# Optimization experiments

Hardware: AMD Instinct MI355X
Metric: run time of the kernel (lower is better)

The kernel has to match this reference:

```python
import jax, jax.numpy as jnp
import numpy as np

B, T, N, HID = 64, 24, 184, 128
IN2 = 2  # 2 * in_dim


def setup_inputs() -> dict:
    key = jax.random.key(0)
    ks = jax.random.split(key, 7)
    s = 1.0 / np.sqrt(HID)
    return {
        "pm25_hist": jax.random.normal(ks[0], (B, T, N, 1), dtype=jnp.float32),
        "W_ih": jax.random.uniform(ks[1], (3 * HID, IN2), dtype=jnp.float32, minval=-s, maxval=s),
        "W_hh": jax.random.uniform(ks[2], (3 * HID, HID), dtype=jnp.float32, minval=-s, maxval=s),
        "b_ih": jax.random.uniform(ks[3], (3 * HID,), dtype=jnp.float32, minval=-s, maxval=s),
        "b_hh": jax.random.uniform(ks[4], (3 * HID,), dtype=jnp.float32, minval=-s, maxval=s),
        "fc_w": jax.random.uniform(ks[5], (1, HID), dtype=jnp.float32, minval=-s, maxval=s),
        "fc_b": jax.random.uniform(ks[6], (1,), dtype=jnp.float32, minval=-s, maxval=s),
    }


def _encoder(pm25_hist, W_ih, W_hh, b_ih, b_hh, fc_w, fc_b):
    b, t, n, _ = pm25_hist.shape
    hid = W_hh.shape[1]
    h0 = jnp.zeros((b * n, hid), dtype=pm25_hist.dtype)
    x0 = jnp.zeros((b, n, 1), dtype=pm25_hist.dtype)
    xs = jnp.transpose(pm25_hist, (1, 0, 2, 3))  # [T, B, N, 1]

    def step(carry, pm_t):
        hn, xn = carry
        x = jnp.concatenate([xn, pm_t], axis=-1).reshape(b * n, -1)  # [B*N, 2]
        gi = x @ W_ih.T + b_ih      # [B*N, 3H]
        gh = hn @ W_hh.T + b_hh     # [B*N, 3H]
        i_r, i_z, i_n = jnp.split(gi, 3, axis=-1)
        h_r, h_z, h_n = jnp.split(gh, 3, axis=-1)
        r = jax.nn.sigmoid(i_r + h_r)
        z = jax.nn.sigmoid(i_z + h_z)
        nt = jnp.tanh(i_n + r * h_n)
        h_new = (1.0 - z) * nt + z * hn
        Ht = h_new.reshape(b, n, hid)
        x_new = Ht @ fc_w.T + fc_b  # [B, N, 1]
        return (h_new, x_new), Ht

    (_, xn_final), H = jax.lax.scan(step, (h0, x0), xs)
    H = jnp.transpose(H, (1, 0, 2, 3))  # [B, T, N, HID]
    return H, xn_final


def reference(pm25_hist, W_ih, W_hh, b_ih, b_hh, fc_w, fc_b):
    return _encoder(pm25_hist, W_ih, W_hh, b_ih, b_hh, fc_w, fc_b)
```

## Files before the change

kernel.cpp:

```cpp
#include <hip/hip_runtime.h>
#include <hip/hip_fp16.h>


#define B_   64
#define T_   24
#define N_   184
#define H_   128
#define BN   (B_ * N_)
#define TN   (T_ * N_)
#define HSZ  (B_ * T_ * N_ * H_)
#define MROWS 16
#define NBLK  (BN / MROWS)
#define S16   136

typedef _Float16 v8h __attribute__((ext_vector_type(8)));
typedef float    v4f __attribute__((ext_vector_type(4)));

static __device__ __forceinline__ float fast_rcp(float x) {
#if __has_builtin(__builtin_amdgcn_rcpf)
    return __builtin_amdgcn_rcpf(x);
#else
    return 1.0f / x;
#endif
}
static __device__ __forceinline__ float sigm_f(float x) {
    return fast_rcp(1.0f + __expf(-x));
}
static __device__ __forceinline__ float tanh_f(float x) {
    return 1.0f - 2.0f * fast_rcp(1.0f + __expf(2.0f * x));
}

__global__ __launch_bounds__(256, 2)
void gru_encoder_kernel(const float* __restrict__ pm,
                        const float* __restrict__ Wih,
                        const float* __restrict__ Whh,
                        const float* __restrict__ bih,
                        const float* __restrict__ bhh,
                        const float* __restrict__ fcw,
                        const float* __restrict__ fcb,
                        float* __restrict__ out)
{
    __shared__ _Float16 hf[MROWS * S16];
    __shared__ float    pml[T_ * MROWS];
    __shared__ float    xlds[MROWS];
    __shared__ float    xpart[4 * MROWS];

    const int tid  = threadIdx.x;
    const int w    = tid >> 6;
    const int lane = tid & 63;
    const int u    = lane & 15;
    const int q    = lane >> 4;

    for (int idx = tid; idx < MROWS * S16; idx += 256) hf[idx] = (_Float16)0.0f;
    if (tid < MROWS) xlds[tid] = 0.0f;

    for (int idx = tid; idx < T_ * MROWS; idx += 256) {
        const int row = idx & (MROWS - 1);
        const int t   = idx >> 4;
        const int g   = blockIdx.x * MROWS + row;
        const int b   = g / N_;
        const int n   = g - b * N_;
        pml[t * MROWS + row] = pm[b * TN + t * N_ + n];
    }

    v8h bfr[3][2][4];
#pragma unroll
    for (int g = 0; g < 3; ++g)
#pragma unroll
        for (int p = 0; p < 2; ++p) {
            const int n = g * 128 + (2 * w + p) * 16 + u;
#pragma unroll
            for (int ks = 0; ks < 4; ++ks) {
                const float* src = Whh + n * 128 + ks * 32 + q * 8;
                v8h hb;
#pragma unroll
                for (int j = 0; j < 8; ++j) hb[j] = (_Float16)src[j];
                bfr[g][p][ks] = hb;
            }
        }

    float w0[3][2], w1[3][2], brz0[2], brz1[2], bin_[2], bhn_[2], fcwr[2];
#pragma unroll
    for (int p = 0; p < 2; ++p) {
        const int i = (2 * w + p) * 16 + u;
        w0[0][p] = Wih[(0 * 128 + i) * 2 + 0];  w1[0][p] = Wih[(0 * 128 + i) * 2 + 1];
        w0[1][p] = Wih[(1 * 128 + i) * 2 + 0];  w1[1][p] = Wih[(1 * 128 + i) * 2 + 1];
        w0[2][p] = Wih[(2 * 128 + i) * 2 + 0];  w1[2][p] = Wih[(2 * 128 + i) * 2 + 1];
        brz0[p] = bih[0 * 128 + i] + bhh[0 * 128 + i];
        brz1[p] = bih[1 * 128 + i] + bhh[1 * 128 + i];
        bin_[p] = bih[2 * 128 + i];
        bhn_[p] = bhh[2 * 128 + i];
        fcwr[p] = fcw[i];
    }
    const float fcbv = fcb[0];

    int obase[4];
#pragma unroll
    for (int reg = 0; reg < 4; ++reg) {
        const int g = blockIdx.x * MROWS + q * 4 + reg;
        const int b = g / N_;
        obase[reg] = b * TN + (g - b * N_);
    }

    v4f hreg[2];
    hreg[0] = (v4f){0.f, 0.f, 0.f, 0.f};
    hreg[1] = (v4f){0.f, 0.f, 0.f, 0.f};

    __syncthreads();

    for (int t = 0; t < T_; ++t) {
        v4f acc[3][2];
#pragma unroll
        for (int g = 0; g < 3; ++g)
#pragma unroll
            for (int p = 0; p < 2; ++p) acc[g][p] = (v4f){0.f, 0.f, 0.f, 0.f};

#pragma unroll
        for (int ks = 0; ks < 4; ++ks) {
            const v8h afr = *(const v8h*)&hf[u * S16 + ks * 32 + q * 8];
#pragma unroll
            for (int g = 0; g < 3; ++g)
#pragma unroll
                for (int p = 0; p < 2; ++p)
                    acc[g][p] = __builtin_amdgcn_mfma_f32_16x16x32_f16(
                        afr, bfr[g][p][ks], acc[g][p], 0, 0, 0);
        }
        __syncthreads();

        const int tN = t * N_;
#pragma unroll
        for (int reg = 0; reg < 4; ++reg) {
            const int lr  = q * 4 + reg;
            const int ob  = obase[reg] + tN;
            const float xp  = xlds[lr];
            const float pmv = pml[t * MROWS + lr];
            float xsum = 0.0f;
#pragma unroll
            for (int p = 0; p < 2; ++p) {
                const int i = (2 * w + p) * 16 + u;
                const float r  = sigm_f(xp * w0[0][p] + pmv * w1[0][p] + acc[0][p][reg] + brz0[p]);
                const float z  = sigm_f(xp * w0[1][p] + pmv * w1[1][p] + acc[1][p][reg] + brz1[p]);
                const float nt = tanh_f(xp * w0[2][p] + pmv * w1[2][p] + bin_[p] +
                                        r * (acc[2][p][reg] + bhn_[p]));
                const float hnew = (1.0f - z) * nt + z * hreg[p][reg];
                hreg[p][reg] = hnew;
                hf[lr * S16 + i] = (_Float16)hnew;
                out[(size_t)ob * H_ + i] = hnew;
                xsum += hnew * fcwr[p];
            }
            xsum += __shfl_xor(xsum, 1, 64);
            xsum += __shfl_xor(xsum, 2, 64);
            xsum += __shfl_xor(xsum, 4, 64);
            xsum += __shfl_xor(xsum, 8, 64);
            if (u == 0) xpart[w * MROWS + lr] = xsum;
        }
        __syncthreads();

        if (tid < MROWS) {
            const float x = xpart[tid] + xpart[MROWS + tid] + xpart[2 * MROWS + tid] +
                            xpart[3 * MROWS + tid] + fcbv;
            xlds[tid] = x;
            if (t == T_ - 1) {
                out[(size_t)HSZ + blockIdx.x * MROWS + tid] = x;
            }
        }
    }
}

extern "C" void kernel_launch(void* const* d_in, const int* in_sizes, int n_in,
                              void* d_out, int out_size, void* d_ws, size_t ws_size,
                              hipStream_t stream) {
    const float* pm  = (const float*)d_in[0];
    const float* Wih = (const float*)d_in[1];
    const float* Whh = (const float*)d_in[2];
    const float* bih = (const float*)d_in[3];
    const float* bhh = (const float*)d_in[4];
    const float* fcw = (const float*)d_in[5];
    const float* fcb = (const float*)d_in[6];
    float* out = (float*)d_out;

    gru_encoder_kernel<<<dim3(NBLK), dim3(256), 0, stream>>>(
        pm, Wih, Whh, bih, bhh, fcw, fcb, out);
}
```

Before: 227.0 us.

## Fold FC feedback into recurrent weights, double-buffer hidden state, widen to 512 threads

The x_t = fc(h_t) feedback into the r and z gates is folded algebraically into W_hh (Whh + Wih0*fcw) and the biases. The n gate's x term is computed by an extra MFMA against fcw, which removes the cross-wave shuffle reduction, the xpart/xlds shared buffers and one barrier per step. The hidden-state LDS tile is double-buffered so only one __syncthreads remains per timestep. Blocks go to 512 threads with one 16-column slice per wave, which raises parallelism per block but also raises the launch-bound occupancy target, and folding in fp16 may change rounding.

```diff
diff --git a/kernel.cpp b/kernel.cpp
--- a/kernel.cpp
+++ b/kernel.cpp
@@ -30,7 +30,7 @@
     return 1.0f - 2.0f * fast_rcp(1.0f + __expf(2.0f * x));
 }
 
-__global__ __launch_bounds__(256, 2)
+__global__ __launch_bounds__(512, 4)
 void gru_encoder_kernel(const float* __restrict__ pm,
                         const float* __restrict__ Wih,
                         const float* __restrict__ Whh,
@@ -40,59 +40,63 @@
                         const float* __restrict__ fcb,
                         float* __restrict__ out)
 {
-    __shared__ _Float16 hf[MROWS * S16];
+    __shared__ _Float16 hf[2][MROWS * S16];
     __shared__ float    pml[T_ * MROWS];
-    __shared__ float    xlds[MROWS];
-    __shared__ float    xpart[4 * MROWS];
 
     const int tid  = threadIdx.x;
     const int w    = tid >> 6;
     const int lane = tid & 63;
     const int u    = lane & 15;
     const int q    = lane >> 4;
+    const int i    = w * 16 + u;
 
-    for (int idx = tid; idx < MROWS * S16; idx += 256) hf[idx] = (_Float16)0.0f;
-    if (tid < MROWS) xlds[tid] = 0.0f;
+    for (int idx = tid; idx < MROWS * S16; idx += 512) hf[0][idx] = (_Float16)0.0f;
 
-    for (int idx = tid; idx < T_ * MROWS; idx += 256) {
+    for (int idx = tid; idx < T_ * MROWS; idx += 512) {
         const int row = idx & (MROWS - 1);
         const int t   = idx >> 4;
         const int g   = blockIdx.x * MROWS + row;
         const int b   = g / N_;
         const int n   = g - b * N_;
-        pml[t * MROWS + row] = pm[b * TN + t * N_ + n];
+        pml[idx] = pm[b * TN + t * N_ + n];
     }
 
-    v8h bfr[3][2][4];
+    v8h bfr[3][4];
 #pragma unroll
-    for (int g = 0; g < 3; ++g)
+    for (int g = 0; g < 3; ++g) {
+        const int c = g * 128 + i;
+        const float fold = (g < 2) ? Wih[c * 2 + 0] : 0.0f;
 #pragma unroll
-        for (int p = 0; p < 2; ++p) {
-            const int n = g * 128 + (2 * w + p) * 16 + u;
+        for (int ks = 0; ks < 4; ++ks) {
+            v8h hb;
 #pragma unroll
-            for (int ks = 0; ks < 4; ++ks) {
-                const float* src = Whh + n * 128 + ks * 32 + q * 8;
-                v8h hb;
+            for (int j = 0; j < 8; ++j) {
+                const int k = ks * 32 + q * 8 + j;
+                hb[j] = (_Float16)(Whh[c * 128 + k] + fold * fcw[k]);
+            }
+            bfr[g][ks] = hb;
+        }
+    }
+    v8h bfx[4];
 #pragma unroll
-                for (int j = 0; j < 8; ++j) hb[j] = (_Float16)src[j];
-                bfr[g][p][ks] = hb;
-            }
-        }
+    for (int ks = 0; ks < 4; ++ks) {
+        v8h hb;
+#pragma unroll
+        for (int j = 0; j < 8; ++j) hb[j] = (_Float16)fcw[ks * 32 + q * 8 + j];
+        bfx[ks] = hb;
+    }
 
-    float w0[3][2], w1[3][2], brz0[2], brz1[2], bin_[2], bhn_[2], fcwr[2];
-#pragma unroll
-    for (int p = 0; p < 2; ++p) {
-        const int i = (2 * w + p) * 16 + u;
-        w0[0][p] = Wih[(0 * 128 + i) * 2 + 0];  w1[0][p] = Wih[(0 * 128 + i) * 2 + 1];
-        w0[1][p] = Wih[(1 * 128 + i) * 2 + 0];  w1[1][p] = Wih[(1 * 128 + i) * 2 + 1];
-        w0[2][p] = Wih[(2 * 128 + i) * 2 + 0];  w1[2][p] = Wih[(2 * 128 + i) * 2 + 1];
-        brz0[p] = bih[0 * 128 + i] + bhh[0 * 128 + i];
-        brz1[p] = bih[1 * 128 + i] + bhh[1 * 128 + i];
-        bin_[p] = bih[2 * 128 + i];
-        bhn_[p] = bhh[2 * 128 + i];
-        fcwr[p] = fcw[i];
-    }
+    const float w1r = Wih[(0 * 128 + i) * 2 + 1];
+    const float w1z = Wih[(1 * 128 + i) * 2 + 1];
+    const float w1n = Wih[(2 * 128 + i) * 2 + 1];
+    const float w0n = Wih[(2 * 128 + i) * 2 + 0];
     const float fcbv = fcb[0];
+    const float brz_r0 = bih[0 * 128 + i] + bhh[0 * 128 + i];
+    const float brz_z0 = bih[1 * 128 + i] + bhh[1 * 128 + i];
+    const float brz_r1 = brz_r0 + Wih[(0 * 128 + i) * 2 + 0] * fcbv;
+    const float brz_z1 = brz_z0 + Wih[(1 * 128 + i) * 2 + 0] * fcbv;
+    const float bin_ = bih[2 * 128 + i];
+    const float bhn_ = bhh[2 * 128 + i];
 
     int obase[4];
 #pragma unroll
@@ -102,67 +106,56 @@
         obase[reg] = b * TN + (g - b * N_);
     }
 
-    v4f hreg[2];
-    hreg[0] = (v4f){0.f, 0.f, 0.f, 0.f};
-    hreg[1] = (v4f){0.f, 0.f, 0.f, 0.f};
+    v4f hreg = (v4f){0.f, 0.f, 0.f, 0.f};
 
     __syncthreads();
 
     for (int t = 0; t < T_; ++t) {
-        v4f acc[3][2];
-#pragma unroll
-        for (int g = 0; g < 3; ++g)
-#pragma unroll
-            for (int p = 0; p < 2; ++p) acc[g][p] = (v4f){0.f, 0.f, 0.f, 0.f};
-
+        const _Float16* hfr = hf[t & 1];
+        v4f acc0 = (v4f){0.f, 0.f, 0.f, 0.f};
+        v4f acc1 = (v4f){0.f, 0.f, 0.f, 0.f};
+        v4f acc2 = (v4f){0.f, 0.f, 0.f, 0.f};
+        v4f accx = (v4f){0.f, 0.f, 0.f, 0.f};
 #pragma unroll
         for (int ks = 0; ks < 4; ++ks) {
-            const v8h afr = *(const v8h*)&hf[u * S16 + ks * 32 + q * 8];
-#pragma unroll
-            for (int g = 0; g < 3; ++g)
-#pragma unroll
-                for (int p = 0; p < 2; ++p)
-                    acc[g][p] = __builtin_amdgcn_mfma_f32_16x16x32_f16(
-                        afr, bfr[g][p][ks], acc[g][p], 0, 0, 0);
+            const v8h afr = *(const v8h*)&hfr[u * S16 + ks * 32 + q * 8];
+            acc0 = __builtin_amdgcn_mfma_f32_16x16x32_f16(afr, bfr[0][ks], acc0, 0, 0, 0);
+            acc1 = __builtin_amdgcn_mfma_f32_16x16x32_f16(afr, bfr[1][ks], acc1, 0, 0, 0);
+            acc2 = __builtin_amdgcn_mfma_f32_16x16x32_f16(afr, bfr[2][ks], acc2, 0, 0, 0);
+            accx = __builtin_amdgcn_mfma_f32_16x16x32_f16(afr, bfx[ks],    accx, 0, 0, 0);
         }
-        __syncthreads();
 
+        _Float16* hfw = hf[(t + 1) & 1];
+        const float brzr = (t == 0) ? brz_r0 : brz_r1;
+        const float brzz = (t == 0) ? brz_z0 : brz_z1;
         const int tN = t * N_;
 #pragma unroll
         for (int reg = 0; reg < 4; ++reg) {
-            const int lr  = q * 4 + reg;
-            const int ob  = obase[reg] + tN;
-            const float xp  = xlds[lr];
+            const int lr   = q * 4 + reg;
             const float pmv = pml[t * MROWS + lr];
-            float xsum = 0.0f;
-#pragma unroll
-            for (int p = 0; p < 2; ++p) {
-                const int i = (2 * w + p) * 16 + u;
-                const float r  = sigm_f(xp * w0[0][p] + pmv * w1[0][p] + acc[0][p][reg] + brz0[p]);
-                const float z  = sigm_f(xp * w0[1][p] + pmv * w1[1][p] + acc[1][p][reg] + brz1[p]);
-                const float nt = tanh_f(xp * w0[2][p] + pmv * w1[2][p] + bin_[p] +
-                                        r * (acc[2][p][reg] + bhn_[p]));
-                const float hnew = (1.0f - z) * nt + z * hreg[p][reg];
-                hreg[p][reg] = hnew;
-                hf[lr * S16 + i] = (_Float16)hnew;
-                out[(size_t)ob * H_ + i] = hnew;
-                xsum += hnew * fcwr[p];
-            }
-            xsum += __shfl_xor(xsum, 1, 64);
-            xsum += __shfl_xor(xsum, 2, 64);
-            xsum += __shfl_xor(xsum, 4, 64);
-            xsum += __shfl_xor(xsum, 8, 64);
-            if (u == 0) xpart[w * MROWS + lr] = xsum;
+            const float xv  = (t == 0) ? 0.0f : (accx[reg] + fcbv);
+            const float r   = sigm_f(acc0[reg] + pmv * w1r + brzr);
+            const float z   = sigm_f(acc1[reg] + pmv * w1z + brzz);
+            const float nt  = tanh_f(xv * w0n + pmv * w1n + bin_ + r * (acc2[reg] + bhn_));
+            const float hnew = nt + z * (hreg[reg] - nt);
+            hreg[reg] = hnew;
+            hfw[lr * S16 + i] = (_Float16)hnew;
+            out[(size_t)(obase[reg] + tN) * H_ + i] = hnew;
         }
         __syncthreads();
+    }
 
-        if (tid < MROWS) {
-            const float x = xpart[tid] + xpart[MROWS + tid] + xpart[2 * MROWS + tid] +
-                            xpart[3 * MROWS + tid] + fcbv;
-            xlds[tid] = x;
-            if (t == T_ - 1) {
-                out[(size_t)HSZ + blockIdx.x * MROWS + tid] = x;
-            }
+    if (w == 0) {
+        v4f accx = (v4f){0.f, 0.f, 0.f, 0.f};
+#pragma unroll
+        for (int ks = 0; ks < 4; ++ks) {
+            const v8h afr = *(const v8h*)&hf[0][u * S16 + ks * 32 + q * 8];
+            accx = __builtin_amdgcn_mfma_f32_16x16x32_f16(afr, bfx[ks], accx, 0, 0, 0);
+        }
+        if (u == 0) {
+#pragma unroll
+            for (int reg = 0; reg < 4; ++reg)
+                out[(size_t)HSZ + blockIdx.x * MROWS + q * 4 + reg] = accx[reg] + fcbv;
         }
     }
 }
@@ -179,6 +172,6 @@
     const float* fcb = (const float*)d_in[6];
     float* out = (float*)d_out;
 
-    gru_encoder_kernel<<<dim3(NBLK), dim3(256), 0, stream>>>(
+    gru_encoder_kernel<<<dim3(NBLK), dim3(512), 0, stream>>>(
         pm, Wih, Whh, bih, bhh, fcw, fcb, out);
 }
```

Result: faster. 203.8 us (-10.2%).
